# Kernel optimization log

Hardware: AMD Instinct MI355X
Metric: run time of the kernel (lower is better)

The kernel has to match this reference:

```python
import jax, jax.numpy as jnp
import numpy as np

M = 100000   # BS*L nodes
D_IN = 256   # in_d
D_OUT = 256  # out_d
E = 1024     # number of edges; indices index the out_d axis (faithful to source quirk)


def setup_inputs() -> dict:
    key = jax.random.key(0)
    k1, k2, k3 = jax.random.split(key, 3)
    node_features = jax.random.normal(k1, (1, M, D_IN), dtype=jnp.float32)
    W = jax.random.normal(k2, (D_OUT, D_IN), dtype=jnp.float32) * (1.0 / np.sqrt(D_IN))
    b = jnp.zeros((D_OUT,), dtype=jnp.float32)
    edge_mapping = jax.random.randint(k3, (2, E), 0, D_OUT, dtype=jnp.int64)
    batch_lens = jnp.ones((M, 1), dtype=jnp.float32)
    return {"node_features": node_features, "W": W, "b": b,
            "edge_mapping": edge_mapping, "batch_lens": batch_lens}


def reference(node_features, W, b, edge_mapping, batch_lens):
    # fc: [1, M, in_d] -> [1, M, out_d]
    h = jnp.einsum('bmi,oi->bmo', node_features, W) + b
    residual = h                              # [1, M, D_OUT]
    hf = jnp.swapaxes(h, 1, 2)[0]             # [D_OUT, M]  (transpose(2,1).squeeze(0))
    gathered = hf[edge_mapping[1]]            # [E, M]      (index_select dim=0)
    agg = jnp.zeros_like(hf).at[edge_mapping[0]].add(gathered)  # scatter-add, [D_OUT, M]
    new_nf = agg.T                            # [M, D_OUT]
    out = (new_nf + residual) / batch_lens    # broadcast -> [1, M, D_OUT]
    return out
```

## Files before the change

kernel.cpp:

```cpp
#include <hip/hip_runtime.h>
#include <cstdint>

constexpr int D = 256;
constexpr int TM = 64;

typedef __bf16 bf16x8 __attribute__((ext_vector_type(8)));
typedef float  f32x4  __attribute__((ext_vector_type(4)));

__global__ void prep_copy(const float* __restrict__ W, const float* __restrict__ b,
                          float* __restrict__ W2, float* __restrict__ b2) {
    int i = blockIdx.x * 256 + threadIdx.x;
    W2[i] = W[i];
    if (blockIdx.x == 0) b2[threadIdx.x] = b[threadIdx.x];
}

__global__ void prep_edges(const int* __restrict__ em, int E,
                           const float* __restrict__ W, const float* __restrict__ b,
                           float* __restrict__ W2, float* __restrict__ b2) {
    int e = blockIdx.x;
    int k = threadIdx.x;
    int dst = em[e];
    int src = em[E + e];
    atomicAdd(&W2[dst * D + k], W[src * D + k]);
    if (k == 0) atomicAdd(&b2[dst], b[src]);
}

__global__ void prep_convert(const float* __restrict__ W2, ushort* __restrict__ Wh,
                             ushort* __restrict__ Wl) {
    int i = blockIdx.x * 256 + threadIdx.x;
    int o = i >> 8, k = i & 255;
    float x = W2[i];
    uint32_t u  = __float_as_uint(x);
    uint32_t hu = u & 0xFFFF0000u;
    float r = x - __uint_as_float(hu);
    uint32_t ru = __float_as_uint(r);
    uint32_t lu = ru + 0x7FFFu + ((ru >> 16) & 1u);
    int kc = k >> 5, kk = k & 31, q = kk >> 3, j = kk & 7;
    int o16b = o >> 4;
    int lane = (o & 15) + 16 * q;
    int idx = kc * 8192 + (o16b * 64 + lane) * 8 + j;
    Wh[idx] = (ushort)(hu >> 16);
    Wl[idx] = (ushort)(lu >> 16);
}

__device__ __forceinline__ void cvt8(const float4& f0, const float4& f1,
                                     uint4& hi, uint4& lo) {
    float xs[8] = {f0.x, f0.y, f0.z, f0.w, f1.x, f1.y, f1.z, f1.w};
    uint32_t h[8], l[8];
    #pragma unroll
    for (int j = 0; j < 8; ++j) {
        uint32_t u  = __float_as_uint(xs[j]);
        uint32_t hu = u & 0xFFFF0000u;
        h[j] = hu;
        float r = xs[j] - __uint_as_float(hu);
        uint32_t ru = __float_as_uint(r);
        l[j] = ru + 0x7FFFu + ((ru >> 16) & 1u);
    }
    hi = make_uint4((h[0] >> 16) | (h[1] & 0xFFFF0000u),
                    (h[2] >> 16) | (h[3] & 0xFFFF0000u),
                    (h[4] >> 16) | (h[5] & 0xFFFF0000u),
                    (h[6] >> 16) | (h[7] & 0xFFFF0000u));
    lo = make_uint4((l[0] >> 16) | (l[1] & 0xFFFF0000u),
                    (l[2] >> 16) | (l[3] & 0xFFFF0000u),
                    (l[4] >> 16) | (l[5] & 0xFFFF0000u),
                    (l[6] >> 16) | (l[7] & 0xFFFF0000u));
}

__global__ __launch_bounds__(256, 3) void resgcn_mfma(
    const float* __restrict__ X, const ushort* __restrict__ Whg,
    const ushort* __restrict__ Wlg, const float* __restrict__ b2,
    const float* __restrict__ blen, float* __restrict__ out, int M)
{
    __shared__ __align__(16) unsigned char smem[16384];
    ushort* XhP = (ushort*)smem;
    ushort* XlP = XhP + 4096;
    float*  E   = (float*)smem;

    const int tid  = threadIdx.x;
    const int lane = tid & 63;
    const int wv   = tid >> 6;
    const int m0   = blockIdx.x * TM;

    const int sm = tid >> 2;
    const int sh = tid & 3;
    int srow = m0 + sm; if (srow >= M) srow = M - 1;
    const float* xrow = X + (size_t)srow * D + sh * 8;
    const int m16b = sm >> 4;
    const int wlane = (sm & 15) + 16 * sh;

    const ushort* whb = Whg + ((wv * 4) * 64 + lane) * 8;
    const ushort* wlb = Wlg + ((wv * 4) * 64 + lane) * 8;

#define LOADW(BH, BL, c) do {                                             \
        _Pragma("unroll")                                                 \
        for (int b = 0; b < 4; ++b) {                                     \
            BH[b] = *(const bf16x8*)(whb + (c) * 8192 + b * 512);         \
            BL[b] = *(const bf16x8*)(wlb + (c) * 8192 + b * 512);         \
        } } while (0)

#define DOMFMA(BH, BL, cur) do {                                          \
        _Pragma("unroll")                                                 \
        for (int a = 0; a < 4; ++a) {                                     \
            bf16x8 ah = *(const bf16x8*)(XhP + (((cur)*4 + a)*64 + lane)*8); \
            bf16x8 al = *(const bf16x8*)(XlP + (((cur)*4 + a)*64 + lane)*8); \
            _Pragma("unroll")                                             \
            for (int b = 0; b < 4; ++b) {                                 \
                acc[a][b] = __builtin_amdgcn_mfma_f32_16x16x32_bf16(ah, BH[b], acc[a][b], 0, 0, 0); \
                acc[a][b] = __builtin_amdgcn_mfma_f32_16x16x32_bf16(al, BH[b], acc[a][b], 0, 0, 0); \
                acc[a][b] = __builtin_amdgcn_mfma_f32_16x16x32_bf16(ah, BL[b], acc[a][b], 0, 0, 0); \
            } } } while (0)

#define STAGEX(nf0, nf1, buf) do {                                        \
        uint4 h_, l_;                                                     \
        cvt8(nf0, nf1, h_, l_);                                           \
        *(uint4*)(XhP + (((buf)*4 + m16b)*64 + wlane)*8) = h_;            \
        *(uint4*)(XlP + (((buf)*4 + m16b)*64 + wlane)*8) = l_;            \
    } while (0)

    f32x4 acc[4][4];
    #pragma unroll
    for (int a = 0; a < 4; ++a)
        #pragma unroll
        for (int b = 0; b < 4; ++b) acc[a][b] = (f32x4){0.f, 0.f, 0.f, 0.f};

    bf16x8 bhA[4], blA[4], bhB[4], blB[4];
    LOADW(bhA, blA, 0);

    {
        float4 f0 = *(const float4*)(xrow + 0);
        float4 f1 = *(const float4*)(xrow + 4);
        STAGEX(f0, f1, 0);
    }
    __syncthreads();

    #pragma unroll
    for (int kc = 0; kc < 8; kc += 2) {
        {
            const float* p = xrow + (kc + 1) * 32;
            float4 nf0 = *(const float4*)(p + 0);
            float4 nf1 = *(const float4*)(p + 4);
            LOADW(bhB, blB, kc + 1);
            DOMFMA(bhA, blA, 0);
            STAGEX(nf0, nf1, 1);
            __syncthreads();
        }
        {
            float4 nf0, nf1;
            if (kc + 2 < 8) {
                const float* p = xrow + (kc + 2) * 32;
                nf0 = *(const float4*)(p + 0);
                nf1 = *(const float4*)(p + 4);
                LOADW(bhA, blA, kc + 2);
            }
            DOMFMA(bhB, blB, 1);
            if (kc + 2 < 8) STAGEX(nf0, nf1, 0);
            __syncthreads();
        }
    }

    const int col = lane & 15;
    const int rq  = lane >> 4;
    float bias[4];
    #pragma unroll
    for (int b = 0; b < 4; ++b) bias[b] = b2[(wv * 4 + b) * 16 + col];

    #pragma unroll
    for (int a = 0; a < 4; ++a) {
        if (a) __syncthreads();
        #pragma unroll
        for (int r = 0; r < 4; ++r) {
            int row = rq * 4 + r;
            int sw  = (row & 7) << 2;
            #pragma unroll
            for (int b = 0; b < 4; ++b) {
                int o = wv * 64 + b * 16 + col;
                E[row * 256 + (o ^ sw)] = acc[a][b][r] + bias[b];
            }
        }
        __syncthreads();
        #pragma unroll
        for (int j = 0; j < 4; ++j) {
            int row = wv * 4 + j;
            int m = m0 + a * 16 + row;
            f32x4 v = *(const f32x4*)&E[row * 256 + ((lane ^ (row & 7)) << 2)];
            if (m < M) {
                float inv = 1.0f / blen[m];
                f32x4 o4 = {v[0] * inv, v[1] * inv, v[2] * inv, v[3] * inv};
                *(f32x4*)&out[(size_t)m * D + lane * 4] = o4;
            }
        }
    }
#undef LOADW
#undef DOMFMA
#undef STAGEX
}

extern "C" void kernel_launch(void* const* d_in, const int* in_sizes, int n_in,
                              void* d_out, int out_size, void* d_ws, size_t ws_size,
                              hipStream_t stream) {
    (void)n_in; (void)out_size; (void)ws_size;
    const float* X  = (const float*)d_in[0];
    const float* W  = (const float*)d_in[1];
    const float* b  = (const float*)d_in[2];
    const int*   em = (const int*)d_in[3];
    const float* bl = (const float*)d_in[4];
    float* out = (float*)d_out;

    const int M = in_sizes[0] / D;
    const int E = in_sizes[3] / 2;

    float*  W2 = (float*)d_ws;
    float*  b2 = W2 + D * D;
    ushort* Wh = (ushort*)(b2 + D);
    ushort* Wl = Wh + D * D;

    prep_copy<<<D * D / 256, 256, 0, stream>>>(W, b, W2, b2);
    prep_edges<<<E, D, 0, stream>>>(em, E, W, b, W2, b2);
    prep_convert<<<D * D / 256, 256, 0, stream>>>(W2, Wh, Wl);

    int mblocks = (M + TM - 1) / TM;
    resgcn_mfma<<<mblocks, 256, 0, stream>>>(X, Wh, Wl, b2, bl, out, M);
}
```

Baseline: 219.1 us.

## Fuse weight prep into one kernel, deepen X prefetch, raise occupancy, nontemporal stores

Merges the three weight-preparation kernels (copy, atomic edge scatter, bf16 split) into a single kernel. Each block owns one output row and scans the edge list from shared memory instead of issuing atomics, which removes two launches and the intermediate W2 buffer. The main GEMM kernel now prefetches X one chunk further ahead, raises the launch_bounds occupancy hint from 3 to 4, and writes output with nontemporal stores. The higher occupancy target may force register spills, and the fused prep kernel does a serial loop over all edges in every block.

```diff
diff --git a/kernel.cpp b/kernel.cpp
--- a/kernel.cpp
+++ b/kernel.cpp
@@ -7,35 +7,33 @@
 typedef __bf16 bf16x8 __attribute__((ext_vector_type(8)));
 typedef float  f32x4  __attribute__((ext_vector_type(4)));
 
-__global__ void prep_copy(const float* __restrict__ W, const float* __restrict__ b,
-                          float* __restrict__ W2, float* __restrict__ b2) {
-    int i = blockIdx.x * 256 + threadIdx.x;
-    W2[i] = W[i];
-    if (blockIdx.x == 0) b2[threadIdx.x] = b[threadIdx.x];
-}
-
-__global__ void prep_edges(const int* __restrict__ em, int E,
-                           const float* __restrict__ W, const float* __restrict__ b,
-                           float* __restrict__ W2, float* __restrict__ b2) {
-    int e = blockIdx.x;
-    int k = threadIdx.x;
-    int dst = em[e];
-    int src = em[E + e];
-    atomicAdd(&W2[dst * D + k], W[src * D + k]);
-    if (k == 0) atomicAdd(&b2[dst], b[src]);
-}
-
-__global__ void prep_convert(const float* __restrict__ W2, ushort* __restrict__ Wh,
-                             ushort* __restrict__ Wl) {
-    int i = blockIdx.x * 256 + threadIdx.x;
-    int o = i >> 8, k = i & 255;
-    float x = W2[i];
-    uint32_t u  = __float_as_uint(x);
+__global__ void prep_fused(const float* __restrict__ W, const float* __restrict__ b,
+                           const int* __restrict__ em, int E,
+                           ushort* __restrict__ Wh, ushort* __restrict__ Wl,
+                           float* __restrict__ b2) {
+    __shared__ int sem[2048];
+    const int o = blockIdx.x;
+    const int t = threadIdx.x;
+    for (int i = t; i < 2 * E; i += 256) sem[i] = em[i];
+    __syncthreads();
+
+    float w = W[o * D + t];
+    float bias = b[o];
+    for (int e = 0; e < E; ++e) {
+        if (sem[e] == o) {
+            int src = sem[E + e];
+            w += W[src * D + t];
+            bias += b[src];
+        }
+    }
+    if (t == 0) b2[o] = bias;
+
+    uint32_t u  = __float_as_uint(w);
     uint32_t hu = u & 0xFFFF0000u;
-    float r = x - __uint_as_float(hu);
+    float r = w - __uint_as_float(hu);
     uint32_t ru = __float_as_uint(r);
     uint32_t lu = ru + 0x7FFFu + ((ru >> 16) & 1u);
-    int kc = k >> 5, kk = k & 31, q = kk >> 3, j = kk & 7;
+    int kc = t >> 5, kk = t & 31, q = kk >> 3, j = kk & 7;
     int o16b = o >> 4;
     int lane = (o & 15) + 16 * q;
     int idx = kc * 8192 + (o16b * 64 + lane) * 8 + j;
@@ -66,7 +64,7 @@
                     (l[6] >> 16) | (l[7] & 0xFFFF0000u));
 }
 
-__global__ __launch_bounds__(256, 3) void resgcn_mfma(
+__global__ __launch_bounds__(256, 4) void resgcn_mfma(
     const float* __restrict__ X, const ushort* __restrict__ Whg,
     const ushort* __restrict__ Wlg, const float* __restrict__ b2,
     const float* __restrict__ blen, float* __restrict__ out, int M)
@@ -124,36 +122,40 @@
         for (int b = 0; b < 4; ++b) acc[a][b] = (f32x4){0.f, 0.f, 0.f, 0.f};
 
     bf16x8 bhA[4], blA[4], bhB[4], blB[4];
+    float4 xA0, xA1, xB0, xB1;
+
     LOADW(bhA, blA, 0);
-
     {
         float4 f0 = *(const float4*)(xrow + 0);
         float4 f1 = *(const float4*)(xrow + 4);
         STAGEX(f0, f1, 0);
     }
+    xA0 = *(const float4*)(xrow + 32);
+    xA1 = *(const float4*)(xrow + 36);
     __syncthreads();
 
     #pragma unroll
     for (int kc = 0; kc < 8; kc += 2) {
         {
-            const float* p = xrow + (kc + 1) * 32;
-            float4 nf0 = *(const float4*)(p + 0);
-            float4 nf1 = *(const float4*)(p + 4);
+            if (kc + 2 < 8) {
+                const float* p = xrow + (kc + 2) * 32;
+                xB0 = *(const float4*)(p + 0);
+                xB1 = *(const float4*)(p + 4);
+            }
             LOADW(bhB, blB, kc + 1);
             DOMFMA(bhA, blA, 0);
-            STAGEX(nf0, nf1, 1);
+            STAGEX(xA0, xA1, 1);
             __syncthreads();
         }
         {
-            float4 nf0, nf1;
-            if (kc + 2 < 8) {
-                const float* p = xrow + (kc + 2) * 32;
-                nf0 = *(const float4*)(p + 0);
-                nf1 = *(const float4*)(p + 4);
-                LOADW(bhA, blA, kc + 2);
-            }
+            if (kc + 3 < 8) {
+                const float* p = xrow + (kc + 3) * 32;
+                xA0 = *(const float4*)(p + 0);
+                xA1 = *(const float4*)(p + 4);
+            }
+            if (kc + 2 < 8) LOADW(bhA, blA, kc + 2);
             DOMFMA(bhB, blB, 1);
-            if (kc + 2 < 8) STAGEX(nf0, nf1, 0);
+            if (kc + 2 < 8) STAGEX(xB0, xB1, 0);
             __syncthreads();
         }
     }
@@ -186,7 +188,7 @@
             if (m < M) {
                 float inv = 1.0f / blen[m];
                 f32x4 o4 = {v[0] * inv, v[1] * inv, v[2] * inv, v[3] * inv};
-                *(f32x4*)&out[(size_t)m * D + lane * 4] = o4;
+                __builtin_nontemporal_store(o4, (f32x4*)&out[(size_t)m * D + lane * 4]);
             }
         }
     }
@@ -209,14 +211,11 @@
     const int M = in_sizes[0] / D;
     const int E = in_sizes[3] / 2;
 
-    float*  W2 = (float*)d_ws;
-    float*  b2 = W2 + D * D;
+    float*  b2 = (float*)d_ws;
     ushort* Wh = (ushort*)(b2 + D);
     ushort* Wl = Wh + D * D;
 
-    prep_copy<<<D * D / 256, 256, 0, stream>>>(W, b, W2, b2);
-    prep_edges<<<E, D, 0, stream>>>(em, E, W, b, W2, b2);
-    prep_convert<<<D * D / 256, 256, 0, stream>>>(W2, Wh, Wl);
+    prep_fused<<<D, 256, 0, stream>>>(W, b, em, E, Wh, Wl, b2);
 
     int mblocks = (M + TM - 1) / TM;
     resgcn_mfma<<<mblocks, 256, 0, stream>>>(X, Wh, Wl, b2, bl, out, M);
```

After: 308.8 us. 1.41x slower.
